# Kernel tuning notes

Measured on AMD Instinct MI355X. Metric: run time of the kernel, lower is better.

Reference implementation:

```python
import jax, jax.numpy as jnp
import numpy as np

B, N, F_IN = 32, 1024, 64   # batch, num_nodes, diffusion_size[0]
K = 3                        # expansion_step
H = 2                        # num_heads
HID, RAW, OUT, CLS = 128, 128, 128, 2
D1, D2 = 128, 128            # diffusion_size[1], diffusion_size[2]
CAT = D1 + RAW               # concat dim fed to attention (h || h_prime) = 256


def setup_inputs() -> dict:
    key = jax.random.key(0)
    ks = jax.random.split(key, 40)
    g = lambda i, shape: jax.random.normal(ks[i], shape, dtype=jnp.float32) * 0.05
    inp = {
        'X': jax.random.normal(ks[0], (B, N, F_IN), dtype=jnp.float32),
        'A': jax.random.uniform(ks[1], (B, N, N), dtype=jnp.float32),
        # transition tensors / mixing weights (only the 2 layers used in forward)
        'T': g(2, (2, K, N, N)),
        'theta': jnp.full((2, K), 1.0 / K, dtype=jnp.float32),
        # raw feature projection
        'W_raw': g(3, (F_IN, RAW)), 'b_raw': jnp.zeros((RAW,), jnp.float32),
        # diffusion layer linears
        'Wd0': g(4, (F_IN, D1)), 'bd0': jnp.zeros((D1,), jnp.float32),
        'Wd1': g(5, (D1, D2)),   'bd1': jnp.zeros((D2,), jnp.float32),
        # final classifier
        'W_fin': g(6, (OUT, CLS)), 'b_fin': jnp.zeros((CLS,), jnp.float32),
    }
    # two CatMultiAttn blocks: q/k/v projections (CAT->HID), out proj (HID->OUT)
    i = 7
    for l in range(2):
        for nm in ('q', 'k', 'v'):
            inp[f'W{nm}{l}'] = g(i, (CAT, HID)); i += 1
            inp[f'b{nm}{l}'] = jnp.zeros((HID,), jnp.float32)
        inp[f'Wo{l}'] = g(i, (HID, OUT)); i += 1
        inp[f'bo{l}'] = jnp.zeros((OUT,), jnp.float32)
    return inp


def _diffusion(theta_l, T_l, h, A, W, b):
    # Q = sum_k theta_k * T_k  (generalized graph diffusion transition)
    Q = jnp.einsum('k,kij->ij', theta_l, T_l)          # [N,N]
    S = Q[None, :, :] * A                               # [B,N,N] mask by adjacency
    z = jnp.einsum('bij,bjf->bif', S, h)                # diffuse features
    return jax.nn.relu(z @ W + b)


def _cat_attn(h, hp, Wq, bq, Wk, bk, Wv, bv, Wo, bo):
    # concatenate diffused + embedding features, multi-head self-attn over nodes
    x = jnp.concatenate([h, hp], axis=-1)               # [B,N,CAT]
    b, n, _ = x.shape
    q = (x @ Wq + bq).reshape(b, n, H, HID // H)
    k = (x @ Wk + bk).reshape(b, n, H, HID // H)
    v = (x @ Wv + bv).reshape(b, n, H, HID // H)
    scale = jnp.asarray(1.0 / np.sqrt(HID // H), x.dtype)
    s = jnp.einsum('bnhd,bmhd->bhnm', q, k) * scale     # [B,H,N,N]
    p = jax.nn.softmax(s, axis=-1)
    ctx = jnp.einsum('bhnm,bmhd->bnhd', p, v).reshape(b, n, HID)
    return jax.nn.relu(ctx @ Wo + bo)


def reference(X, A, T, theta, W_raw, b_raw, Wd0, bd0, Wd1, bd1,
              W_fin, b_fin,
              Wq0, bq0, Wk0, bk0, Wv0, bv0, Wo0, bo0,
              Wq1, bq1, Wk1, bk1, Wv1, bv1, Wo1, bo1):
    theta_soft = jax.nn.softmax(theta, axis=-1)         # [2,K]
    h_prime = X @ W_raw + b_raw                          # [B,N,RAW]
    # layer 0
    h = _diffusion(theta_soft[0], T[0], X, A, Wd0, bd0)  # [B,N,D1]
    h_prime = _cat_attn(h, h_prime, Wq0, bq0, Wk0, bk0, Wv0, bv0, Wo0, bo0)
    # layer 1 (residual fusion)
    h = _diffusion(theta_soft[1], T[1], h, A, Wd1, bd1)  # [B,N,D2]
    h_prime = h_prime + _cat_attn(h, h_prime, Wq1, bq1, Wk1, bk1, Wv1, bv1, Wo1, bo1)
    return h_prime @ W_fin + b_fin                       # [B,N,CLS]
```

## Files before the change

### kernel.cpp

```cpp
#include <hip/hip_runtime.h>
#include <hip/hip_bf16.h>

typedef __hip_bfloat16 bf16;
typedef __attribute__((ext_vector_type(8))) short s8b;
typedef __attribute__((ext_vector_type(4))) short s4b;
typedef __attribute__((ext_vector_type(4))) float f4;

#define BB   32
#define NN   1024
#define FIN  64
#define HEADS 2
#define DH   64
#define HIDD 128
#define SZQ  ((size_t)BB * NN * HIDD)

__device__ __forceinline__ ushort f2bf(float x) {
    bf16 h = __float2bfloat16(x);
    return *(ushort*)&h;
}
__device__ __forceinline__ float bfbits2f(ushort h) {
    union { uint u; float f; } c; c.u = (uint)h << 16; return c.f;
}
__device__ __forceinline__ uint pk_bf16(float lo, float hi) {
    return (uint)f2bf(lo) | ((uint)f2bf(hi) << 16);
}
union U8 { short s[8]; s8b v; };
union U4 { short s[4]; s4b v; };
union UQ { ushort u[8]; s8b v; };

__global__ __launch_bounds__(256) void setup_kernel(
        const float* __restrict__ raw, const float* __restrict__ d0,
        const float* __restrict__ d1,
        const float* __restrict__ q0w, const float* __restrict__ k0w,
        const float* __restrict__ v0w, const float* __restrict__ o0w,
        const float* __restrict__ q1w, const float* __restrict__ k1w,
        const float* __restrict__ v1w, const float* __restrict__ o1w,
        ushort* __restrict__ Whi, ushort* __restrict__ Wlo,
        const float* __restrict__ T, const float* __restrict__ theta,
        ushort* __restrict__ Q0hi, ushort* __restrict__ Q0lo,
        ushort* __restrict__ Q1hi, ushort* __restrict__ Q1lo,
        const float* __restrict__ X,
        ushort* __restrict__ XT_hi, ushort* __restrict__ XT_lo) {
    __shared__ float tile[64][65];
    const int bid = blockIdx.x;
    const int t = threadIdx.x;
    if (bid < 1024) {
        int id = bid * 256 + t;
        const float* src; int K, off;
        if      (id <   8192) { src = raw; K =  64; off = 0; }
        else if (id <  16384) { src = d0;  K =  64; off = 8192; }
        else if (id <  32768) { src = d1;  K = 128; off = 16384; }
        else if (id <  65536) { src = q0w; K = 256; off = 32768; }
        else if (id <  98304) { src = k0w; K = 256; off = 65536; }
        else if (id < 131072) { src = v0w; K = 256; off = 98304; }
        else if (id < 147456) { src = o0w; K = 128; off = 131072; }
        else if (id < 180224) { src = q1w; K = 256; off = 147456; }
        else if (id < 212992) { src = k1w; K = 256; off = 180224; }
        else if (id < 245760) { src = v1w; K = 256; off = 212992; }
        else                  { src = o1w; K = 128; off = 245760; }
        int il = id - off;
        int k = il >> 7, c = il & 127;
        float w = src[il];
        ushort h = f2bf(w);
        Whi[off + c * K + k] = h;
        Wlo[off + c * K + k] = f2bf(w - bfbits2f(h));
    } else if (bid < 1536) {
        const int tb = bid - 1024;
        const int b  = tb >> 4;
        const int n0 = (tb & 15) * 64;
        {
            int nl = t >> 2, f0 = (t & 3) * 16;
            const float* xp = X + ((size_t)b * NN + n0 + nl) * 64 + f0;
#pragma unroll
            for (int i = 0; i < 16; i += 4)
                *(float4*)&tile[nl][f0 + i] = *(const float4*)(xp + i);
        }
        __syncthreads();
        {
            int f = t >> 2, n1 = (t & 3) * 16;
            U8 h0, h1, l0, l1;
#pragma unroll
            for (int i = 0; i < 16; i++) {
                float v = tile[n1 + i][f];
                ushort hh = f2bf(v);
                ushort ll = f2bf(v - bfbits2f(hh));
                if (i < 8) { h0.s[i] = (short)hh; l0.s[i] = (short)ll; }
                else       { h1.s[i - 8] = (short)hh; l1.s[i - 8] = (short)ll; }
            }
            size_t gb = ((size_t)b * 64 + f) * NN + n0 + n1;
            *(s8b*)&XT_hi[gb]     = h0.v;  *(s8b*)&XT_hi[gb + 8] = h1.v;
            *(s8b*)&XT_lo[gb]     = l0.v;  *(s8b*)&XT_lo[gb + 8] = l1.v;
        }
    } else {
        const int layer = (bid < 2048) ? 0 : 1;
        ushort* Qhi = layer ? Q1hi : Q0hi;
        ushort* Qlo = layer ? Q1lo : Q0lo;
        float t0 = theta[layer * 3 + 0];
        float t1 = theta[layer * 3 + 1];
        float t2 = theta[layer * 3 + 2];
        float m  = fmaxf(t0, fmaxf(t1, t2));
        float e0 = expf(t0 - m), e1 = expf(t1 - m), e2 = expf(t2 - m);
        float inv = 1.0f / (e0 + e1 + e2);
        e0 *= inv; e1 *= inv; e2 *= inv;
        size_t base = ((size_t)((bid - 1536) & 511) * 256 + t) * 8;
        const float* Tl = T + (size_t)layer * 3 * NN * NN;
        U8 hi, lo;
#pragma unroll
        for (int i = 0; i < 8; i++) {
            float q = e0 * Tl[base + i]
                    + e1 * Tl[base + i + (size_t)NN * NN]
                    + e2 * Tl[base + i + (size_t)2 * NN * NN];
            ushort hh = f2bf(q);
            hi.s[i] = (short)hh;
            lo.s[i] = (short)f2bf(q - bfbits2f(hh));
        }
        *(s8b*)&Qhi[base] = hi.v;
        *(s8b*)&Qlo[base] = lo.v;
    }
}

template<int F, bool WRITE_HT>
__global__ __launch_bounds__(512, 4) void diff_dense_kernel(
        const ushort* __restrict__ Qhi, const ushort* __restrict__ Qlo,
        const float* __restrict__ A,
        const ushort* __restrict__ hT_hi, const ushort* __restrict__ hT_lo,
        const ushort* __restrict__ WT_hi, const ushort* __restrict__ WT_lo,
        const float* __restrict__ bias,
        float* __restrict__ hout,
        ushort* __restrict__ hiT, ushort* __restrict__ loT) {
    constexpr int SS  = 72;
    constexpr int NT  = F / 16;
    constexpr int NCW = NT / 4;
    constexpr int SZ2 = F + 8;
    constexpr int P1 = 2 * 64 * SS + 2 * F * SS;
    constexpr int P2 = 2 * 64 * SZ2 + 2 * 128 * 40;
    __shared__ short smem[(P1 > P2) ? P1 : P2];
    short* Shi = smem;
    short* Slo = Shi + 64 * SS;
    short* Hhi = Slo + 64 * SS;
    short* Hlo = Hhi + (size_t)F * SS;
    short* Zhi = smem;
    short* Zlo = Zhi + 64 * SZ2;
    short* Wsh = Zlo + 64 * SZ2;
    short* Wsl = Wsh + 128 * 40;

    const int bidx = blockIdx.x;
    const int u  = bidx >> 3;
    const int b  = (bidx & 7) + 8 * (u >> 4);
    const int i0 = (u & 15) * 64;
    const int t  = threadIdx.x;
    const int w  = t >> 6, lane = t & 63;
    const int quad = lane >> 4, c = lane & 15;
    const int rh = w >> 2;
    const int ch = w & 3;

    const int srow = t >> 3, scol = (t & 7) * 8;
    const float*  Ap = A   + ((size_t)b * NN + i0 + srow) * NN + scol;
    const ushort* Qh = Qhi + (size_t)(i0 + srow) * NN + scol;
    const ushort* Ql = Qlo + (size_t)(i0 + srow) * NN + scol;
    constexpr int HTR = 512 / F;
    constexpr int HJ  = 64 / HTR;
    constexpr int HV  = HJ / 8;
    const int hrow = t / HTR, hcol = (t % HTR) * HJ;
    const ushort* Hh = hT_hi + ((size_t)b * F + hrow) * NN + hcol;
    const ushort* Hl = hT_lo + ((size_t)b * F + hrow) * NN + hcol;

    f4 acc[2][NCW];
#pragma unroll
    for (int st = 0; st < 2; st++)
#pragma unroll
        for (int i = 0; i < NCW; i++) acc[st][i] = (f4){0.f, 0.f, 0.f, 0.f};

    float4 a0 = *(const float4*)Ap, a1 = *(const float4*)(Ap + 4);
    s8b hhv[HV], hlv[HV];
#pragma unroll
    for (int vv = 0; vv < HV; vv++) {
        hhv[vv] = *(const s8b*)(Hh + 8 * vv);
        hlv[vv] = *(const s8b*)(Hl + 8 * vv);
    }

#pragma unroll 1
    for (int j0 = 0; j0 < NN; j0 += 64) {
        UQ qh, ql;
        qh.v = *(const s8b*)(Qh + j0);
        ql.v = *(const s8b*)(Ql + j0);
        __syncthreads();
        {
            float av[8] = {a0.x, a0.y, a0.z, a0.w, a1.x, a1.y, a1.z, a1.w};
            U8 hi, lo;
#pragma unroll
            for (int i = 0; i < 8; i++) {
                float q = bfbits2f(qh.u[i]) + bfbits2f(ql.u[i]);
                float s = q * av[i];
                ushort hb = f2bf(s);
                hi.s[i] = (short)hb;
                lo.s[i] = (short)f2bf(s - bfbits2f(hb));
            }
            *(s8b*)&Shi[srow * SS + scol] = hi.v;
            *(s8b*)&Slo[srow * SS + scol] = lo.v;
#pragma unroll
            for (int vv = 0; vv < HV; vv++) {
                *(s8b*)&Hhi[hrow * SS + hcol + 8 * vv] = hhv[vv];
                *(s8b*)&Hlo[hrow * SS + hcol + 8 * vv] = hlv[vv];
            }
        }
        if (j0 + 64 < NN) {
            a0 = *(const float4*)(Ap + j0 + 64);
            a1 = *(const float4*)(Ap + j0 + 68);
#pragma unroll
            for (int vv = 0; vv < HV; vv++) {
                hhv[vv] = *(const s8b*)(Hh + j0 + 64 + 8 * vv);
                hlv[vv] = *(const s8b*)(Hl + j0 + 64 + 8 * vv);
            }
        }
        __syncthreads();

#pragma unroll
        for (int ks = 0; ks < 2; ks++) {
            s8b ah0 = *(const s8b*)&Shi[(32 * rh + c) * SS + ks * 32 + quad * 8];
            s8b al0 = *(const s8b*)&Slo[(32 * rh + c) * SS + ks * 32 + quad * 8];
            s8b ah1 = *(const s8b*)&Shi[(32 * rh + 16 + c) * SS + ks * 32 + quad * 8];
            s8b al1 = *(const s8b*)&Slo[(32 * rh + 16 + c) * SS + ks * 32 + quad * 8];
#pragma unroll
            for (int ctn = 0; ctn < NCW; ctn++) {
                const int nt = ch * NCW + ctn;
                s8b bhi = *(const s8b*)&Hhi[(nt * 16 + c) * SS + ks * 32 + quad * 8];
                s8b blo = *(const s8b*)&Hlo[(nt * 16 + c) * SS + ks * 32 + quad * 8];
                acc[0][ctn] = __builtin_amdgcn_mfma_f32_16x16x32_bf16(ah0, bhi, acc[0][ctn], 0, 0, 0);
                acc[0][ctn] = __builtin_amdgcn_mfma_f32_16x16x32_bf16(al0, bhi, acc[0][ctn], 0, 0, 0);
                acc[0][ctn] = __builtin_amdgcn_mfma_f32_16x16x32_bf16(ah0, blo, acc[0][ctn], 0, 0, 0);
                acc[1][ctn] = __builtin_amdgcn_mfma_f32_16x16x32_bf16(ah1, bhi, acc[1][ctn], 0, 0, 0);
                acc[1][ctn] = __builtin_amdgcn_mfma_f32_16x16x32_bf16(al1, bhi, acc[1][ctn], 0, 0, 0);
                acc[1][ctn] = __builtin_amdgcn_mfma_f32_16x16x32_bf16(ah1, blo, acc[1][ctn], 0, 0, 0);
            }
        }
    }

    __syncthreads();
#pragma unroll
    for (int st = 0; st < 2; st++)
#pragma unroll
        for (int ctn = 0; ctn < NCW; ctn++)
#pragma unroll
            for (int r = 0; r < 4; r++) {
                const int row = 32 * rh + 16 * st + quad * 4 + r;
                const int col = (ch * NCW + ctn) * 16 + c;
                float v = acc[st][ctn][r];
                ushort hh = f2bf(v);
                Zhi[row * SZ2 + col] = (short)hh;
                Zlo[row * SZ2 + col] = (short)f2bf(v - bfbits2f(hh));
            }

    const int rh2 = w >> 2;
    const int ch2 = w & 3;
    f4 acc2[2][2];
#pragma unroll
    for (int st = 0; st < 2; st++)
#pragma unroll
        for (int i = 0; i < 2; i++) acc2[st][i] = (f4){0.f, 0.f, 0.f, 0.f};

    constexpr int NKT = F / 32;
    for (int kt = 0; kt < NKT; kt++) {
        __syncthreads();
        {
            int cc = t >> 2, kk = (t & 3) * 8;
            size_t gsrc = (size_t)cc * F + kt * 32 + kk;
            *(s8b*)&Wsh[cc * 40 + kk] = *(const s8b*)&WT_hi[gsrc];
            *(s8b*)&Wsl[cc * 40 + kk] = *(const s8b*)&WT_lo[gsrc];
        }
        __syncthreads();

        s8b ah0 = *(const s8b*)&Zhi[(32 * rh2 + c) * SZ2 + kt * 32 + quad * 8];
        s8b al0 = *(const s8b*)&Zlo[(32 * rh2 + c) * SZ2 + kt * 32 + quad * 8];
        s8b ah1 = *(const s8b*)&Zhi[(32 * rh2 + 16 + c) * SZ2 + kt * 32 + quad * 8];
        s8b al1 = *(const s8b*)&Zlo[(32 * rh2 + 16 + c) * SZ2 + kt * 32 + quad * 8];
#pragma unroll
        for (int ct = 0; ct < 2; ct++) {
            s8b bh = *(const s8b*)&Wsh[(ch2 * 32 + ct * 16 + c) * 40 + quad * 8];
            s8b bl = *(const s8b*)&Wsl[(ch2 * 32 + ct * 16 + c) * 40 + quad * 8];
            acc2[0][ct] = __builtin_amdgcn_mfma_f32_16x16x32_bf16(ah0, bh, acc2[0][ct], 0, 0, 0);
            acc2[0][ct] = __builtin_amdgcn_mfma_f32_16x16x32_bf16(al0, bh, acc2[0][ct], 0, 0, 0);
            acc2[0][ct] = __builtin_amdgcn_mfma_f32_16x16x32_bf16(ah0, bl, acc2[0][ct], 0, 0, 0);
            acc2[1][ct] = __builtin_amdgcn_mfma_f32_16x16x32_bf16(ah1, bh, acc2[1][ct], 0, 0, 0);
            acc2[1][ct] = __builtin_amdgcn_mfma_f32_16x16x32_bf16(al1, bh, acc2[1][ct], 0, 0, 0);
            acc2[1][ct] = __builtin_amdgcn_mfma_f32_16x16x32_bf16(ah1, bl, acc2[1][ct], 0, 0, 0);
        }
    }

#pragma unroll
    for (int st = 0; st < 2; st++) {
        const int rg0 = i0 + 32 * rh2 + 16 * st + quad * 4;
#pragma unroll
        for (int ct = 0; ct < 2; ct++) {
            const int col = ch2 * 32 + ct * 16 + c;
            float bv = bias[col];
            float vv[4];
#pragma unroll
            for (int r = 0; r < 4; r++) {
                float v = fmaxf(acc2[st][ct][r] + bv, 0.f);
                hout[((size_t)b * NN + rg0 + r) * 128 + col] = v;
                vv[r] = v;
            }
            if (WRITE_HT) {
                U4 ph, pl;
#pragma unroll
                for (int r = 0; r < 4; r++) {
                    ushort hh = f2bf(vv[r]);
                    ph.s[r] = (short)hh;
                    pl.s[r] = (short)f2bf(vv[r] - bfbits2f(hh));
                }
                size_t tb = ((size_t)b * 128 + col) * NN + rg0;
                *(s4b*)&hiT[tb] = ph.v;
                *(s4b*)&loT[tb] = pl.v;
            }
        }
    }
}

template<int K1, int K2, int CB, bool RELU, bool RESID, int OMODE>
__global__ __launch_bounds__(512) void dense_mfma_kernel(
        const float* __restrict__ in1, const float* __restrict__ in2,
        const ushort* __restrict__ WT_hi, const ushort* __restrict__ WT_lo,
        const float* __restrict__ bias, const float* __restrict__ biask,
        const float* __restrict__ biasv,
        float* __restrict__ out, ushort* __restrict__ outq) {
    constexpr int KD  = K1 + K2;
    constexpr int NKT = KD / 32;
    constexpr int NCH = CB / 32;
    __shared__ short Xhi[128][40], Xlo[128][40];
    __shared__ short Whi[CB][40], Wlo[CB][40];

    int bx, by;
    if (OMODE == 1) {
        const int xcd = blockIdx.x & 7, qq = blockIdx.x >> 3;
        by = qq & 1;
        bx = ((qq >> 1) << 3) | xcd;
    } else { bx = blockIdx.x; by = blockIdx.y; }
    const int r0 = bx * 128;
    const int c0 = by * CB;
    const int t  = threadIdx.x;
    const int w  = t >> 6, lane = t & 63;
    const int quad = lane >> 4, c = lane & 15;
    const int rh = w >> 1;
    const int ch = w & 1;

    f4 acc[2][NCH];
#pragma unroll
    for (int st = 0; st < 2; st++)
#pragma unroll
        for (int i = 0; i < NCH; i++) acc[st][i] = (f4){0.f, 0.f, 0.f, 0.f};

    for (int kt = 0; kt < NKT; kt++) {
        const int k0 = kt * 32;
        __syncthreads();
        {
            int row = t >> 2, kk = (t & 3) * 8;
            int g = r0 + row;
            const float* p;
            if (K2 > 0) {
                int k = k0 + kk;
                p = (k < K1) ? (in1 + (size_t)g * K1 + k)
                             : (in2 + (size_t)g * K2 + (k - K1));
            } else {
                p = in1 + (size_t)g * K1 + k0 + kk;
            }
            float4 a = *(const float4*)p, bq = *(const float4*)(p + 4);
            float sv[8] = {a.x, a.y, a.z, a.w, bq.x, bq.y, bq.z, bq.w};
            U8 hi, lo;
#pragma unroll
            for (int i = 0; i < 8; i++) {
                ushort hh = f2bf(sv[i]);
                hi.s[i] = (short)hh;
                lo.s[i] = (short)f2bf(sv[i] - bfbits2f(hh));
            }
            *(s8b*)&Xhi[row][kk] = hi.v;
            *(s8b*)&Xlo[row][kk] = lo.v;
        }
        {
            for (int id = t; id < CB * 4; id += 512) {
                int cc = id >> 2, kk = (id & 3) * 8;
                size_t gsrc = (size_t)(c0 + cc) * KD + k0 + kk;
                *(s8b*)&Whi[cc][kk] = *(const s8b*)&WT_hi[gsrc];
                *(s8b*)&Wlo[cc][kk] = *(const s8b*)&WT_lo[gsrc];
            }
        }
        __syncthreads();

        s8b ah0 = *(const s8b*)&Xhi[32 * rh + c][quad * 8];
        s8b al0 = *(const s8b*)&Xlo[32 * rh + c][quad * 8];
        s8b ah1 = *(const s8b*)&Xhi[32 * rh + 16 + c][quad * 8];
        s8b al1 = *(const s8b*)&Xlo[32 * rh + 16 + c][quad * 8];
#pragma unroll
        for (int ct = 0; ct < NCH; ct++) {
            s8b bh = *(const s8b*)&Whi[ch * (CB / 2) + ct * 16 + c][quad * 8];
            s8b bl = *(const s8b*)&Wlo[ch * (CB / 2) + ct * 16 + c][quad * 8];
            acc[0][ct] = __builtin_amdgcn_mfma_f32_16x16x32_bf16(ah0, bh, acc[0][ct], 0, 0, 0);
            acc[0][ct] = __builtin_amdgcn_mfma_f32_16x16x32_bf16(al0, bh, acc[0][ct], 0, 0, 0);
            acc[0][ct] = __builtin_amdgcn_mfma_f32_16x16x32_bf16(ah0, bl, acc[0][ct], 0, 0, 0);
            acc[1][ct] = __builtin_amdgcn_mfma_f32_16x16x32_bf16(ah1, bh, acc[1][ct], 0, 0, 0);
            acc[1][ct] = __builtin_amdgcn_mfma_f32_16x16x32_bf16(al1, bh, acc[1][ct], 0, 0, 0);
            acc[1][ct] = __builtin_amdgcn_mfma_f32_16x16x32_bf16(ah1, bl, acc[1][ct], 0, 0, 0);
        }
    }

#pragma unroll
    for (int st = 0; st < 2; st++) {
        const int row_g0 = r0 + 32 * rh + 16 * st + quad * 4;
#pragma unroll
        for (int ct = 0; ct < NCH; ct++) {
            const int col = c0 + ch * (CB / 2) + ct * 16 + c;
            if (OMODE == 1) {
                int tensor = col >> 7, cc2 = col & 127;
                float bv = (tensor == 0 ? bias : tensor == 1 ? biask : biasv)[cc2];
                int head = cc2 >> 6, d = cc2 & 63;
                int b = row_g0 >> 10, n = row_g0 & 1023;
                if (tensor == 2) {
                    U4 pk;
#pragma unroll
                    for (int r = 0; r < 4; r++) pk.s[r] = (short)f2bf(acc[st][ct][r] + bv);
                    size_t addr = (((size_t)b * HEADS + head) * 64 + d) * NN + n;
                    *(s4b*)&outq[2 * SZQ + addr] = pk.v;
                } else {
                    ushort* dst = outq + (size_t)tensor * SZQ
                                + (((size_t)b * HEADS + head) * NN + n) * 64 + d;
#pragma unroll
                    for (int r = 0; r < 4; r++) dst[(size_t)r * 64] = f2bf(acc[st][ct][r] + bv);
                }
            } else {
                float bv = bias[col];
#pragma unroll
                for (int r = 0; r < 4; r++) {
                    float v = acc[st][ct][r] + bv;
                    if (RELU) v = fmaxf(v, 0.f);
                    size_t o = (size_t)(row_g0 + r) * 128 + col;
                    if (RESID) v += out[o];
                    out[o] = v;
                }
            }
        }
    }
}

template<bool FINAL>
__global__ __launch_bounds__(512) void attn_oproj_kernel(
        const ushort* __restrict__ q, const ushort* __restrict__ k,
        const ushort* __restrict__ vt,
        const ushort* __restrict__ WoT_hi, const ushort* __restrict__ WoT_lo,
        const float* __restrict__ bo,
        float* __restrict__ hp,
        const float* __restrict__ Wfin, const float* __restrict__ bfin,
        float* __restrict__ fout) {
    constexpr int ZS = 136;
    constexpr int PB = 2 * 128 * ZS + 2 * 128 * 40 + 512;
    __shared__ short smem[PB];
    short* Ks  = smem;
    short* Vt  = smem + 128 * 72;
    short* Zhi = smem;
    short* Zlo = Zhi + 128 * ZS;
    short* Wsh = Zlo + 128 * ZS;
    short* Wsl = Wsh + 128 * 40;
    float* red = (float*)(Wsl + 128 * 40);

    const int bidx = blockIdx.x;
    const int u  = bidx >> 3;
    const int b  = (bidx & 7) + 8 * (u >> 3);
    const int n0 = (u & 7) * 128;
    const int t  = threadIdx.x;
    const int w  = t >> 6;
    const int lane = t & 63;
    const int quad = lane >> 4, c = lane & 15;
    const float scale = 0.125f;

    const int skey = t >> 2, sd0 = (t & 3) * 16;
    const int svd  = t >> 3, svc = (t & 7) * 16;

    f4 Oh[2][4];
    float li[2];

#pragma unroll
    for (int h = 0; h < 2; h++) {
        const size_t kvbase = ((size_t)(b * HEADS + h)) * NN * 64;
        s8b qf0, qf1;
        {
            const ushort* qrow = q + kvbase + (size_t)(n0 + 16 * w + c) * 64;
            qf0 = *(const s8b*)(qrow + quad * 8);
            qf1 = *(const s8b*)(qrow + 32 + quad * 8);
        }
        f4 O[4];
#pragma unroll
        for (int i = 0; i < 4; i++) O[i] = (f4){0.f, 0.f, 0.f, 0.f};
        float l_i = 0.f;

        for (int kt0 = 0; kt0 < NN; kt0 += 128) {
            __syncthreads();
            {
                const ushort* kr = k + kvbase + (size_t)(kt0 + skey) * 64 + sd0;
                *(s8b*)&Ks[skey * 72 + sd0]     = *(const s8b*)kr;
                *(s8b*)&Ks[skey * 72 + sd0 + 8] = *(const s8b*)(kr + 8);
                const ushort* vr = vt + kvbase + (size_t)svd * NN + kt0 + svc;
                *(s8b*)&Vt[svd * 136 + svc]     = *(const s8b*)vr;
                *(s8b*)&Vt[svd * 136 + svc + 8] = *(const s8b*)(vr + 8);
            }
            __syncthreads();

            f4 sg[4][2];
#pragma unroll
            for (int g = 0; g < 4; g++) {
                const int kb = g * 32;
                sg[g][0] = (f4){0.f, 0.f, 0.f, 0.f};
                sg[g][1] = (f4){0.f, 0.f, 0.f, 0.f};
#pragma unroll
                for (int ck = 0; ck < 2; ck++) {
                    s8b ka = *(const s8b*)&Ks[(kb + c) * 72 + ck * 32 + quad * 8];
                    s8b kB = *(const s8b*)&Ks[(kb + 16 + c) * 72 + ck * 32 + quad * 8];
                    s8b qf = ck ? qf1 : qf0;
                    sg[g][0] = __builtin_amdgcn_mfma_f32_16x16x32_bf16(ka, qf, sg[g][0], 0, 0, 0);
                    sg[g][1] = __builtin_amdgcn_mfma_f32_16x16x32_bf16(kB, qf, sg[g][1], 0, 0, 0);
                }
            }
            float pv[4][8];
            float ps = 0.f;
#pragma unroll
            for (int g = 0; g < 4; g++)
#pragma unroll
                for (int r = 0; r < 4; r++) {
                    pv[g][r]     = __expf(sg[g][0][r] * scale);
                    pv[g][4 + r] = __expf(sg[g][1][r] * scale);
                    ps += pv[g][r] + pv[g][4 + r];
                }
            ps += __shfl_xor(ps, 16);
            ps += __shfl_xor(ps, 32);
            l_i += ps;

            int addr0 = ((((2 * quad) & 3) << 4) | c) << 2;
            int addr1 = ((((2 * quad + 1) & 3) << 4) | c) << 2;
            int tsel = quad >> 1;
#pragma unroll
            for (int g = 0; g < 4; g++) {
                const int kb = g * 32;
                uint Da01 = pk_bf16(pv[g][0], pv[g][1]), Da23 = pk_bf16(pv[g][2], pv[g][3]);
                uint Db01 = pk_bf16(pv[g][4], pv[g][5]), Db23 = pk_bf16(pv[g][6], pv[g][7]);
                int A01_0 = __builtin_amdgcn_ds_bpermute(addr0, (int)Da01);
                int A23_0 = __builtin_amdgcn_ds_bpermute(addr0, (int)Da23);
                int B01_0 = __builtin_amdgcn_ds_bpermute(addr0, (int)Db01);
                int B23_0 = __builtin_amdgcn_ds_bpermute(addr0, (int)Db23);
                int A01_1 = __builtin_amdgcn_ds_bpermute(addr1, (int)Da01);
                int A23_1 = __builtin_amdgcn_ds_bpermute(addr1, (int)Da23);
                int B01_1 = __builtin_amdgcn_ds_bpermute(addr1, (int)Db01);
                int B23_1 = __builtin_amdgcn_ds_bpermute(addr1, (int)Db23);
                union { int i[4]; s8b s; } pf;
                pf.i[0] = tsel ? B01_0 : A01_0;
                pf.i[1] = tsel ? B23_0 : A23_0;
                pf.i[2] = tsel ? B01_1 : A01_1;
                pf.i[3] = tsel ? B23_1 : A23_1;
#pragma unroll
                for (int dt = 0; dt < 4; dt++) {
                    s8b vf = *(const s8b*)&Vt[(16 * dt + c) * 136 + kb + quad * 8];
                    O[dt] = __builtin_amdgcn_mfma_f32_16x16x32_bf16(vf, pf.s, O[dt], 0, 0, 0);
                }
            }
        }
        li[h] = 1.0f / l_i;
#pragma unroll
        for (int dt = 0; dt < 4; dt++) Oh[h][dt] = O[dt];
    }

    __syncthreads();
    {
        const int zrow = 16 * w + c;
#pragma unroll
        for (int h = 0; h < 2; h++) {
            float inv = li[h];
#pragma unroll
            for (int dt = 0; dt < 4; dt++) {
                U4 ph, pl;
#pragma unroll
                for (int r = 0; r < 4; r++) {
                    float v = Oh[h][dt][r] * inv;
                    ushort hh = f2bf(v);
                    ph.s[r] = (short)hh;
                    pl.s[r] = (short)f2bf(v - bfbits2f(hh));
                }
                int col = h * 64 + 16 * dt + 4 * quad;
                *(s4b*)&Zhi[zrow * ZS + col] = ph.v;
                *(s4b*)&Zlo[zrow * ZS + col] = pl.v;
            }
        }
    }

    const int rh = w >> 1;
    const int ch = w & 1;
    f4 acc[2][4];
#pragma unroll
    for (int st = 0; st < 2; st++)
#pragma unroll
        for (int i = 0; i < 4; i++) acc[st][i] = (f4){0.f, 0.f, 0.f, 0.f};

    for (int kt = 0; kt < 4; kt++) {
        __syncthreads();
        {
            int cc = t >> 2, kk = (t & 3) * 8;
            size_t gsrc = (size_t)cc * 128 + kt * 32 + kk;
            *(s8b*)&Wsh[cc * 40 + kk] = *(const s8b*)&WoT_hi[gsrc];
            *(s8b*)&Wsl[cc * 40 + kk] = *(const s8b*)&WoT_lo[gsrc];
        }
        __syncthreads();

        s8b ah0 = *(const s8b*)&Zhi[(32 * rh + c) * ZS + kt * 32 + quad * 8];
        s8b al0 = *(const s8b*)&Zlo[(32 * rh + c) * ZS + kt * 32 + quad * 8];
        s8b ah1 = *(const s8b*)&Zhi[(32 * rh + 16 + c) * ZS + kt * 32 + quad * 8];
        s8b al1 = *(const s8b*)&Zlo[(32 * rh + 16 + c) * ZS + kt * 32 + quad * 8];
#pragma unroll
        for (int ct = 0; ct < 4; ct++) {
            s8b bh = *(const s8b*)&Wsh[(ch * 64 + ct * 16 + c) * 40 + quad * 8];
            s8b bl = *(const s8b*)&Wsl[(ch * 64 + ct * 16 + c) * 40 + quad * 8];
            acc[0][ct] = __builtin_amdgcn_mfma_f32_16x16x32_bf16(ah0, bh, acc[0][ct], 0, 0, 0);
            acc[0][ct] = __builtin_amdgcn_mfma_f32_16x16x32_bf16(al0, bh, acc[0][ct], 0, 0, 0);
            acc[0][ct] = __builtin_amdgcn_mfma_f32_16x16x32_bf16(ah0, bl, acc[0][ct], 0, 0, 0);
            acc[1][ct] = __builtin_amdgcn_mfma_f32_16x16x32_bf16(ah1, bh, acc[1][ct], 0, 0, 0);
            acc[1][ct] = __builtin_amdgcn_mfma_f32_16x16x32_bf16(al1, bh, acc[1][ct], 0, 0, 0);
            acc[1][ct] = __builtin_amdgcn_mfma_f32_16x16x32_bf16(ah1, bl, acc[1][ct], 0, 0, 0);
        }
    }

    if (FINAL) {
        float fc[2][2][4];
#pragma unroll
        for (int st = 0; st < 2; st++)
#pragma unroll
            for (int o = 0; o < 2; o++)
#pragma unroll
                for (int r = 0; r < 4; r++) fc[st][o][r] = 0.f;
#pragma unroll
        for (int ct = 0; ct < 4; ct++) {
            const int col = ch * 64 + ct * 16 + c;
            float bv = bo[col];
            float w0 = Wfin[col * 2], w1 = Wfin[col * 2 + 1];
#pragma unroll
            for (int st = 0; st < 2; st++) {
                const size_t rg = (size_t)b * NN + n0 + 32 * rh + 16 * st + quad * 4;
#pragma unroll
                for (int r = 0; r < 4; r++) {
                    float v = fmaxf(acc[st][ct][r] + bv, 0.f);
                    v += hp[(rg + r) * 128 + col];
                    fc[st][0][r] += v * w0;
                    fc[st][1][r] += v * w1;
                }
            }
        }
#pragma unroll
        for (int st = 0; st < 2; st++)
#pragma unroll
            for (int r = 0; r < 4; r++) {
                float a0 = fc[st][0][r], a1 = fc[st][1][r];
#pragma unroll
                for (int off = 1; off < 16; off <<= 1) {
                    a0 += __shfl_xor(a0, off, 16);
                    a1 += __shfl_xor(a1, off, 16);
                }
                fc[st][0][r] = a0; fc[st][1][r] = a1;
            }
        if (ch == 1 && c == 0) {
#pragma unroll
            for (int st = 0; st < 2; st++)
#pragma unroll
                for (int r = 0; r < 4; r++) {
                    int lr = 32 * rh + 16 * st + quad * 4 + r;
                    red[lr * 2]     = fc[st][0][r];
                    red[lr * 2 + 1] = fc[st][1][r];
                }
        }
        __syncthreads();
        if (ch == 0 && c == 0) {
#pragma unroll
            for (int st = 0; st < 2; st++)
#pragma unroll
                for (int r = 0; r < 4; r++) {
                    int lr = 32 * rh + 16 * st + quad * 4 + r;
                    size_t row = (size_t)b * NN + n0 + lr;
                    fout[row * 2]     = fc[st][0][r] + red[lr * 2]     + bfin[0];
                    fout[row * 2 + 1] = fc[st][1][r] + red[lr * 2 + 1] + bfin[1];
                }
        }
        return;
    }

#pragma unroll
    for (int st = 0; st < 2; st++) {
        const size_t rg = (size_t)b * NN + n0 + 32 * rh + 16 * st + quad * 4;
#pragma unroll
        for (int ct = 0; ct < 4; ct++) {
            const int col = ch * 64 + ct * 16 + c;
            float bv = bo[col];
#pragma unroll
            for (int r = 0; r < 4; r++)
                hp[(rg + r) * 128 + col] = fmaxf(acc[st][ct][r] + bv, 0.f);
        }
    }
}

extern "C" void kernel_launch(void* const* d_in, const int* in_sizes, int n_in,
                              void* d_out, int out_size, void* d_ws, size_t ws_size,
                              hipStream_t stream) {
    (void)in_sizes; (void)n_in; (void)out_size; (void)ws_size;
    const float* X     = (const float*)d_in[0];
    const float* A     = (const float*)d_in[1];
    const float* T     = (const float*)d_in[2];
    const float* theta = (const float*)d_in[3];
    const float* W_raw = (const float*)d_in[4];
    const float* b_raw = (const float*)d_in[5];
    const float* Wd0   = (const float*)d_in[6];
    const float* bd0   = (const float*)d_in[7];
    const float* Wd1   = (const float*)d_in[8];
    const float* bd1   = (const float*)d_in[9];
    const float* W_fin = (const float*)d_in[10];
    const float* b_fin = (const float*)d_in[11];
    const float* Wq0 = (const float*)d_in[12]; const float* bq0 = (const float*)d_in[13];
    const float* Wk0 = (const float*)d_in[14]; const float* bk0 = (const float*)d_in[15];
    const float* Wv0 = (const float*)d_in[16]; const float* bv0 = (const float*)d_in[17];
    const float* Wo0 = (const float*)d_in[18]; const float* bo0 = (const float*)d_in[19];
    const float* Wq1 = (const float*)d_in[20]; const float* bq1 = (const float*)d_in[21];
    const float* Wk1 = (const float*)d_in[22]; const float* bk1 = (const float*)d_in[23];
    const float* Wv1 = (const float*)d_in[24]; const float* bv1 = (const float*)d_in[25];
    const float* Wo1 = (const float*)d_in[26]; const float* bo1 = (const float*)d_in[27];

    float* ws   = (float*)d_ws;
    const size_t SZ = (size_t)BB * NN * HIDD;
    ushort* Q0hi = (ushort*)ws;
    ushort* Q0lo = Q0hi + (size_t)NN * NN;
    float* hp   = ws + (size_t)NN * NN;
    float* h    = hp + SZ;
    float* z    = h + SZ;
    ushort* qb  = (ushort*)(z + SZ);
    ushort* kb  = qb + SZ;
    ushort* XT_hi = qb + 3 * SZ;
    ushort* XT_lo = XT_hi + SZ / 2;
    ushort* hT_hi = XT_lo + SZ / 2;
    ushort* hT_lo = hT_hi + SZ;
    ushort* WT_hi = hT_lo + SZ;
    ushort* WT_lo = WT_hi + 262144;
    ushort* Q1hi = WT_lo + 262144;
    ushort* Q1lo = Q1hi + (size_t)NN * NN;

    const int OFF_RAW = 0, OFF_D0 = 8192, OFF_D1 = 16384, OFF_QKV0 = 32768,
              OFF_O0 = 131072, OFF_QKV1 = 147456, OFF_O1 = 245760;

    const int attnGrid = BB * (NN / 128);
    const int diffGrid = BB * (NN / 64);
    const dim3 dg1(256, 1);

    setup_kernel<<<2560, 256, 0, stream>>>(W_raw, Wd0, Wd1, Wq0, Wk0, Wv0, Wo0,
                                           Wq1, Wk1, Wv1, Wo1, WT_hi, WT_lo,
                                           T, theta, Q0hi, Q0lo, Q1hi, Q1lo,
                                           X, XT_hi, XT_lo);

    dense_mfma_kernel<64, 0, 128, false, false, 0><<<dg1, 512, 0, stream>>>(
        X, nullptr, WT_hi + OFF_RAW, WT_lo + OFF_RAW, b_raw, nullptr, nullptr,
        hp, nullptr);
    diff_dense_kernel<64, true><<<diffGrid, 512, 0, stream>>>(
        Q0hi, Q0lo, A, XT_hi, XT_lo, WT_hi + OFF_D0, WT_lo + OFF_D0, bd0,
        h, hT_hi, hT_lo);
    dense_mfma_kernel<128, 128, 192, false, false, 1><<<512, 512, 0, stream>>>(
        h, hp, WT_hi + OFF_QKV0, WT_lo + OFF_QKV0, bq0, bk0, bv0,
        nullptr, qb);
    attn_oproj_kernel<false><<<attnGrid, 512, 0, stream>>>(
        qb, kb, qb + 2 * SZ, WT_hi + OFF_O0, WT_lo + OFF_O0, bo0,
        hp, nullptr, nullptr, nullptr);

    diff_dense_kernel<128, false><<<diffGrid, 512, 0, stream>>>(
        Q1hi, Q1lo, A, hT_hi, hT_lo, WT_hi + OFF_D1, WT_lo + OFF_D1, bd1,
        h, nullptr, nullptr);
    dense_mfma_kernel<128, 128, 192, false, false, 1><<<512, 512, 0, stream>>>(
        h, hp, WT_hi + OFF_QKV1, WT_lo + OFF_QKV1, bq1, bk1, bv1,
        nullptr, qb);
    attn_oproj_kernel<true><<<attnGrid, 512, 0, stream>>>(
        qb, kb, qb + 2 * SZ, WT_hi + OFF_O1, WT_lo + OFF_O1, bo1,
        hp, W_fin, b_fin, (float*)d_out);
}
```

Before: 487.1 us.

## Register-prefetch next global tiles across diffusion, dense and attention kernels

Applies register double-buffering to the diffusion, dense, attention and output-projection loops. The next iteration's global loads (Q, A, H, weights, K/V) are issued after the shared-memory store barrier, so they overlap the current MFMA work instead of sitting between syncs. In attention, the first K/V tile of head 1 is also prefetched during the last tile of head 0. This costs extra registers per thread, which may lower occupancy.

```diff
diff --git a/kernel.cpp b/kernel.cpp
--- a/kernel.cpp
+++ b/kernel.cpp
@@ -178,12 +178,12 @@
         hhv[vv] = *(const s8b*)(Hh + 8 * vv);
         hlv[vv] = *(const s8b*)(Hl + 8 * vv);
     }
+    UQ qh, ql;
+    qh.v = *(const s8b*)Qh;
+    ql.v = *(const s8b*)Ql;
 
 #pragma unroll 1
     for (int j0 = 0; j0 < NN; j0 += 64) {
-        UQ qh, ql;
-        qh.v = *(const s8b*)(Qh + j0);
-        ql.v = *(const s8b*)(Ql + j0);
         __syncthreads();
         {
             float av[8] = {a0.x, a0.y, a0.z, a0.w, a1.x, a1.y, a1.z, a1.w};
@@ -204,6 +204,8 @@
                 *(s8b*)&Hlo[hrow * SS + hcol + 8 * vv] = hlv[vv];
             }
         }
+        __syncthreads();
+
         if (j0 + 64 < NN) {
             a0 = *(const float4*)(Ap + j0 + 64);
             a1 = *(const float4*)(Ap + j0 + 68);
@@ -212,8 +214,9 @@
                 hhv[vv] = *(const s8b*)(Hh + j0 + 64 + 8 * vv);
                 hlv[vv] = *(const s8b*)(Hl + j0 + 64 + 8 * vv);
             }
-        }
-        __syncthreads();
+            qh.v = *(const s8b*)(Qh + j0 + 64);
+            ql.v = *(const s8b*)(Ql + j0 + 64);
+        }
 
 #pragma unroll
         for (int ks = 0; ks < 2; ks++) {
@@ -260,15 +263,19 @@
         for (int i = 0; i < 2; i++) acc2[st][i] = (f4){0.f, 0.f, 0.f, 0.f};
 
     constexpr int NKT = F / 32;
+    const int wcc = t >> 2, wkk = (t & 3) * 8;
+    s8b pwh = *(const s8b*)&WT_hi[(size_t)wcc * F + wkk];
+    s8b pwl = *(const s8b*)&WT_lo[(size_t)wcc * F + wkk];
     for (int kt = 0; kt < NKT; kt++) {
         __syncthreads();
-        {
-            int cc = t >> 2, kk = (t & 3) * 8;
-            size_t gsrc = (size_t)cc * F + kt * 32 + kk;
-            *(s8b*)&Wsh[cc * 40 + kk] = *(const s8b*)&WT_hi[gsrc];
-            *(s8b*)&Wsl[cc * 40 + kk] = *(const s8b*)&WT_lo[gsrc];
-        }
-        __syncthreads();
+        *(s8b*)&Wsh[wcc * 40 + wkk] = pwh;
+        *(s8b*)&Wsl[wcc * 40 + wkk] = pwl;
+        __syncthreads();
+        if (kt + 1 < NKT) {
+            size_t gsrc = (size_t)wcc * F + (kt + 1) * 32 + wkk;
+            pwh = *(const s8b*)&WT_hi[gsrc];
+            pwl = *(const s8b*)&WT_lo[gsrc];
+        }
 
         s8b ah0 = *(const s8b*)&Zhi[(32 * rh2 + c) * SZ2 + kt * 32 + quad * 8];
         s8b al0 = *(const s8b*)&Zlo[(32 * rh2 + c) * SZ2 + kt * 32 + quad * 8];
@@ -327,6 +334,8 @@
     constexpr int KD  = K1 + K2;
     constexpr int NKT = KD / 32;
     constexpr int NCH = CB / 32;
+    constexpr int WCH = CB * 4;
+    constexpr int WPT = (WCH + 511) / 512;
     __shared__ short Xhi[128][40], Xlo[128][40];
     __shared__ short Whi[CB][40], Wlo[CB][40];
 
@@ -350,22 +359,39 @@
 #pragma unroll
         for (int i = 0; i < NCH; i++) acc[st][i] = (f4){0.f, 0.f, 0.f, 0.f};
 
+    const int xrow = t >> 2, xkk = (t & 3) * 8;
+    float4 pa, pbq;
+    s8b pwh[WPT], pwl[WPT];
+    auto loadX = [&](int k0) {
+        int g = r0 + xrow;
+        const float* p;
+        if (K2 > 0) {
+            int k = k0 + xkk;
+            p = (k < K1) ? (in1 + (size_t)g * K1 + k)
+                         : (in2 + (size_t)g * K2 + (k - K1));
+        } else {
+            p = in1 + (size_t)g * K1 + k0 + xkk;
+        }
+        pa = *(const float4*)p; pbq = *(const float4*)(p + 4);
+    };
+    auto loadW = [&](int k0) {
+#pragma unroll
+        for (int i = 0; i < WPT; i++) {
+            int id = t + i * 512;
+            if ((WCH % 512 == 0) || id < WCH) {
+                int cc = id >> 2, kk = (id & 3) * 8;
+                size_t gsrc = (size_t)(c0 + cc) * KD + k0 + kk;
+                pwh[i] = *(const s8b*)&WT_hi[gsrc];
+                pwl[i] = *(const s8b*)&WT_lo[gsrc];
+            }
+        }
+    };
+    loadX(0); loadW(0);
+
     for (int kt = 0; kt < NKT; kt++) {
-        const int k0 = kt * 32;
         __syncthreads();
         {
-            int row = t >> 2, kk = (t & 3) * 8;
-            int g = r0 + row;
-            const float* p;
-            if (K2 > 0) {
-                int k = k0 + kk;
-                p = (k < K1) ? (in1 + (size_t)g * K1 + k)
-                             : (in2 + (size_t)g * K2 + (k - K1));
-            } else {
-                p = in1 + (size_t)g * K1 + k0 + kk;
-            }
-            float4 a = *(const float4*)p, bq = *(const float4*)(p + 4);
-            float sv[8] = {a.x, a.y, a.z, a.w, bq.x, bq.y, bq.z, bq.w};
+            float sv[8] = {pa.x, pa.y, pa.z, pa.w, pbq.x, pbq.y, pbq.z, pbq.w};
             U8 hi, lo;
 #pragma unroll
             for (int i = 0; i < 8; i++) {
@@ -373,18 +399,22 @@
                 hi.s[i] = (short)hh;
                 lo.s[i] = (short)f2bf(sv[i] - bfbits2f(hh));
             }
-            *(s8b*)&Xhi[row][kk] = hi.v;
-            *(s8b*)&Xlo[row][kk] = lo.v;
+            *(s8b*)&Xhi[xrow][xkk] = hi.v;
+            *(s8b*)&Xlo[xrow][xkk] = lo.v;
         }
         {
-            for (int id = t; id < CB * 4; id += 512) {
-                int cc = id >> 2, kk = (id & 3) * 8;
-                size_t gsrc = (size_t)(c0 + cc) * KD + k0 + kk;
-                *(s8b*)&Whi[cc][kk] = *(const s8b*)&WT_hi[gsrc];
-                *(s8b*)&Wlo[cc][kk] = *(const s8b*)&WT_lo[gsrc];
-            }
-        }
-        __syncthreads();
+#pragma unroll
+            for (int i = 0; i < WPT; i++) {
+                int id = t + i * 512;
+                if ((WCH % 512 == 0) || id < WCH) {
+                    int cc = id >> 2, kk = (id & 3) * 8;
+                    *(s8b*)&Whi[cc][kk] = pwh[i];
+                    *(s8b*)&Wlo[cc][kk] = pwl[i];
+                }
+            }
+        }
+        __syncthreads();
+        if (kt + 1 < NKT) { loadX(kt * 32 + 32); loadW(kt * 32 + 32); }
 
         s8b ah0 = *(const s8b*)&Xhi[32 * rh + c][quad * 8];
         s8b al0 = *(const s8b*)&Xlo[32 * rh + c][quad * 8];
@@ -474,6 +504,16 @@
     const int skey = t >> 2, sd0 = (t & 3) * 16;
     const int svd  = t >> 3, svc = (t & 7) * 16;
 
+    s8b pk0, pk1, pv0, pv1;
+    auto loadKV = [&](size_t base, int kt0) {
+        const ushort* kr = k + base + (size_t)(kt0 + skey) * 64 + sd0;
+        pk0 = *(const s8b*)kr;
+        pk1 = *(const s8b*)(kr + 8);
+        const ushort* vr = vt + base + (size_t)svd * NN + kt0 + svc;
+        pv0 = *(const s8b*)vr;
+        pv1 = *(const s8b*)(vr + 8);
+    };
+
     f4 Oh[2][4];
     float li[2];
 
@@ -486,6 +526,7 @@
             qf0 = *(const s8b*)(qrow + quad * 8);
             qf1 = *(const s8b*)(qrow + 32 + quad * 8);
         }
+        if (h == 0) loadKV(kvbase, 0);
         f4 O[4];
 #pragma unroll
         for (int i = 0; i < 4; i++) O[i] = (f4){0.f, 0.f, 0.f, 0.f};
@@ -494,14 +535,14 @@
         for (int kt0 = 0; kt0 < NN; kt0 += 128) {
             __syncthreads();
             {
-                const ushort* kr = k + kvbase + (size_t)(kt0 + skey) * 64 + sd0;
-                *(s8b*)&Ks[skey * 72 + sd0]     = *(const s8b*)kr;
-                *(s8b*)&Ks[skey * 72 + sd0 + 8] = *(const s8b*)(kr + 8);
-                const ushort* vr = vt + kvbase + (size_t)svd * NN + kt0 + svc;
-                *(s8b*)&Vt[svd * 136 + svc]     = *(const s8b*)vr;
-                *(s8b*)&Vt[svd * 136 + svc + 8] = *(const s8b*)(vr + 8);
+                *(s8b*)&Ks[skey * 72 + sd0]     = pk0;
+                *(s8b*)&Ks[skey * 72 + sd0 + 8] = pk1;
+                *(s8b*)&Vt[svd * 136 + svc]     = pv0;
+                *(s8b*)&Vt[svd * 136 + svc + 8] = pv1;
             }
             __syncthreads();
+            if (kt0 + 128 < NN)      loadKV(kvbase, kt0 + 128);
+            else if (h == 0)         loadKV(kvbase + (size_t)NN * 64, 0);
 
             f4 sg[4][2];
 #pragma unroll
@@ -596,15 +637,19 @@
 #pragma unroll
         for (int i = 0; i < 4; i++) acc[st][i] = (f4){0.f, 0.f, 0.f, 0.f};
 
+    const int occ = t >> 2, okk = (t & 3) * 8;
+    s8b owh = *(const s8b*)&WoT_hi[(size_t)occ * 128 + okk];
+    s8b owl = *(const s8b*)&WoT_lo[(size_t)occ * 128 + okk];
     for (int kt = 0; kt < 4; kt++) {
         __syncthreads();
-        {
-            int cc = t >> 2, kk = (t & 3) * 8;
-            size_t gsrc = (size_t)cc * 128 + kt * 32 + kk;
-            *(s8b*)&Wsh[cc * 40 + kk] = *(const s8b*)&WoT_hi[gsrc];
-            *(s8b*)&Wsl[cc * 40 + kk] = *(const s8b*)&WoT_lo[gsrc];
-        }
-        __syncthreads();
+        *(s8b*)&Wsh[occ * 40 + okk] = owh;
+        *(s8b*)&Wsl[occ * 40 + okk] = owl;
+        __syncthreads();
+        if (kt + 1 < 4) {
+            size_t gsrc = (size_t)occ * 128 + (kt + 1) * 32 + okk;
+            owh = *(const s8b*)&WoT_hi[gsrc];
+            owl = *(const s8b*)&WoT_lo[gsrc];
+        }
 
         s8b ah0 = *(const s8b*)&Zhi[(32 * rh + c) * ZS + kt * 32 + quad * 8];
         s8b al0 = *(const s8b*)&Zlo[(32 * rh + c) * ZS + kt * 32 + quad * 8];
```

Result: no change. 490.5 us (+0.7%).
